# Performance work log

Hardware: AMD Instinct MI355X
Metric: run time of the kernel (lower is better)

Reference implementation:

```python
import jax, jax.numpy as jnp
import numpy as np


def setup_inputs() -> dict:
    key = jax.random.key(0)
    ks = jax.random.split(key, 6)
    B, S, H, F, E = 4, 2048, 1024, 4096, 8
    x = jax.random.normal(ks[0], (B, S, H), dtype=jnp.float32)
    Wr = jax.random.normal(ks[1], (H, E), dtype=jnp.float32) * (1.0 / np.sqrt(H))
    br = jnp.zeros((E,), dtype=jnp.float32)
    W1 = jax.random.normal(ks[2], (E, H, F), dtype=jnp.float32) * (1.0 / np.sqrt(H))
    b1 = jnp.zeros((E, F), dtype=jnp.float32)
    W2 = jax.random.normal(ks[3], (E, F, H), dtype=jnp.float32) * (1.0 / np.sqrt(F))
    b2 = jnp.zeros((E, H), dtype=jnp.float32)
    b_buf = jnp.zeros((E,), dtype=jnp.float32)  # load-balancing bias buffer, zero-init
    return {"x": x, "b_buf": b_buf, "Wr": Wr, "br": br,
            "W1": W1, "b1": b1, "W2": W2, "b2": b2, "k": 2}


def reference(x, b_buf, Wr, br, W1, b1, W2, b2, k):
    # Router
    scores = jnp.einsum('bsh,he->bse', x, Wr) + br          # [B,S,E]
    probs = jax.nn.softmax(scores, axis=-1)
    # load_balancing: expert selection uses biased scores (b_buf pre-update)
    _, expert_id = jax.lax.top_k(probs + b_buf, k)          # [B,S,k] int
    # combine weights use unbiased probs
    p, _ = jax.lax.top_k(probs, k)                          # [B,S,k]
    # Dense-dispatch reference: run every expert MLP on all tokens,
    # then select via one-hot mask (same math as gather/scatter dispatch).
    h1 = jnp.einsum('bsh,ehf->ebsf', x, W1) + b1[:, None, None, :]
    h1 = jax.nn.gelu(h1, approximate=False)                 # torch nn.GELU = exact
    out_e = jnp.einsum('ebsf,efh->ebsh', h1, W2) + b2[:, None, None, :]
    E = W1.shape[0]
    onehot = (expert_id[None, :, :, :] == jnp.arange(E)[:, None, None, None]).astype(x.dtype)  # [E,B,S,k]
    out_k = jnp.einsum('ebsk,ebsh->bskh', onehot, out_e)    # scatter-combine per slot
    w = p / jnp.sum(p, axis=-1, keepdims=True)              # normalize top-k probs
    return jnp.einsum('bsk,bskh->bsh', w, out_k)
```

## Files before the change

### kernel.cpp

```cpp
#include <hip/hip_runtime.h>
#include <stdint.h>

#define NTOK 8192
#define H_ 1024
#define F_ 4096
#define E_ 8
#define VCAP 18432
#define VMBLK 72
#define MT 144
#define NCOMP 16384

using f32x4  = __attribute__((ext_vector_type(4))) float;
using short8 = __attribute__((ext_vector_type(8))) short;

typedef __attribute__((address_space(1))) const uint32_t gu32;
typedef __attribute__((address_space(3))) uint32_t lu32;

__device__ __forceinline__ void glds16(const void* g, void* l) {
  __builtin_amdgcn_global_load_lds((gu32*)g, (lu32*)l, 16, 0, 0);
}

__device__ __forceinline__ ushort f2bf(float f) {
  union { float f; uint32_t u; } v; v.f = f;
  uint32_t r = (v.u + 0x7FFFu + ((v.u >> 16) & 1u)) >> 16;
  return (ushort)r;
}

__device__ __forceinline__ float gelu_t(float x) {
  float u = 0.7978845608028654f * (x + 0.044715f * x * x * x);
  float e = exp2f(u * 2.885390081777927f);
  float th = 1.0f - 2.0f / (1.0f + e);
  return 0.5f * x * (1.0f + th);
}

__global__ void k_init(int* cnt, int* cur, int* tok, float* wl, int* v2c) {
  int i = blockIdx.x * 256 + threadIdx.x;
  if (i < E_) { cnt[i] = 0; cur[i] = 0; }
  if (i < VCAP) { tok[i] = -1; wl[i] = 0.f; v2c[i] = -1; }
}

__global__ __launch_bounds__(256) void k_transcvt(const float* __restrict__ W,
                                                  ushort* __restrict__ WT,
                                                  int R, int C) {
  __shared__ float t[64][65];
  int e = blockIdx.z;
  int c0 = blockIdx.x * 64, r0 = blockIdx.y * 64;
  const float* Wp = W + (size_t)e * R * C;
  ushort* Tp = WT + (size_t)e * R * C;
  int tx = threadIdx.x & 15, ty = threadIdx.x >> 4;
#pragma unroll
  for (int i = 0; i < 4; i++) {
    int lr = ty + i * 16;
    const float4 v = *(const float4*)&Wp[(size_t)(r0 + lr) * C + c0 + tx * 4];
    t[lr][tx * 4 + 0] = v.x; t[lr][tx * 4 + 1] = v.y;
    t[lr][tx * 4 + 2] = v.z; t[lr][tx * 4 + 3] = v.w;
  }
  __syncthreads();
#pragma unroll
  for (int i = 0; i < 4; i++) {
    int lc = ty + i * 16;
    ushort4 o;
    o.x = f2bf(t[tx * 4 + 0][lc]);
    o.y = f2bf(t[tx * 4 + 1][lc]);
    o.z = f2bf(t[tx * 4 + 2][lc]);
    o.w = f2bf(t[tx * 4 + 3][lc]);
    *(ushort4*)&Tp[(size_t)(c0 + lc) * R + r0 + tx * 4] = o;
  }
}

__global__ __launch_bounds__(256) void k_router(const float* __restrict__ x,
                                                const float* __restrict__ Wr,
                                                const float* __restrict__ br,
                                                const float* __restrict__ bbuf,
                                                int* cnt, int* te, float* tw) {
  int wid = threadIdx.x >> 6, lane = threadIdx.x & 63;
  int t = blockIdx.x * 4 + wid;
  const float* xp = x + (size_t)t * H_;
  double acc[E_];
#pragma unroll
  for (int e = 0; e < E_; e++) acc[e] = 0.0;
  for (int j = lane; j < H_; j += 64) {
    float xv = xp[j];
    const float4 w0 = *(const float4*)&Wr[j * 8];
    const float4 w1 = *(const float4*)&Wr[j * 8 + 4];
    acc[0] += (double)xv * (double)w0.x;
    acc[1] += (double)xv * (double)w0.y;
    acc[2] += (double)xv * (double)w0.z;
    acc[3] += (double)xv * (double)w0.w;
    acc[4] += (double)xv * (double)w1.x;
    acc[5] += (double)xv * (double)w1.y;
    acc[6] += (double)xv * (double)w1.z;
    acc[7] += (double)xv * (double)w1.w;
  }
#pragma unroll
  for (int e = 0; e < E_; e++)
    for (int s = 32; s > 0; s >>= 1) acc[e] += __shfl_xor(acc[e], s);
  if (lane == 0) {
    double s[E_], m = -1e300;
    for (int e = 0; e < E_; e++) { s[e] = acc[e] + (double)br[e]; if (s[e] > m) m = s[e]; }
    double pe[E_], sum = 0.0;
    for (int e = 0; e < E_; e++) { pe[e] = exp(s[e] - m); sum += pe[e]; }
    double pr[E_], bb[E_];
    for (int e = 0; e < E_; e++) { pr[e] = pe[e] / sum; bb[e] = pr[e] + (double)bbuf[e]; }
    int e0 = 0;
    for (int e = 1; e < E_; e++) if (bb[e] > bb[e0]) e0 = e;
    int e1 = (e0 == 0) ? 1 : 0;
    for (int e = 0; e < E_; e++) if (e != e0 && bb[e] > bb[e1]) e1 = e;
    int a0 = 0;
    for (int e = 1; e < E_; e++) if (pr[e] > pr[a0]) a0 = e;
    int a1 = (a0 == 0) ? 1 : 0;
    for (int e = 0; e < E_; e++) if (e != a0 && pr[e] > pr[a1]) a1 = e;
    double iv = 1.0 / (pr[a0] + pr[a1]);
    te[t * 2] = e0; te[t * 2 + 1] = e1;
    tw[t * 2] = (float)(pr[a0] * iv); tw[t * 2 + 1] = (float)(pr[a1] * iv);
    atomicAdd(&cnt[e0], 1); atomicAdd(&cnt[e1], 1);
  }
}

__global__ void k_offsets(const int* cnt, int* off, int* coff) {
  if (threadIdx.x == 0 && blockIdx.x == 0) {
    int o = 0, c = 0;
    for (int e = 0; e < E_; e++) {
      off[e] = o; coff[e] = c;
      o += ((cnt[e] + 255) >> 8) << 8;
      c += cnt[e];
    }
    off[E_] = o; coff[E_] = c;
  }
}

__global__ void k_build(const int* __restrict__ te, const float* __restrict__ tw,
                        const int* __restrict__ off, const int* __restrict__ coff,
                        int* cur, int* tok, float* wl, int* v2c, int* ctok) {
  int t = blockIdx.x * 256 + threadIdx.x;
  if (t >= NTOK) return;
#pragma unroll
  for (int s = 0; s < 2; s++) {
    int e = te[t * 2 + s];
    int slot = atomicAdd(&cur[e], 1);
    int vp = off[e] + slot;
    int cp = coff[e] + slot;
    tok[vp] = t; wl[vp] = tw[t * 2 + s]; v2c[vp] = cp; ctok[cp] = t;
  }
}

__global__ __launch_bounds__(256) void k_gather(const float* __restrict__ x,
                                                const int* __restrict__ ctok,
                                                ushort* __restrict__ Xg) {
  int row = blockIdx.x;
  int t = ctok[row];
  const float4* src = (const float4*)(x + (size_t)t * H_);
  ushort4* dst = (ushort4*)(Xg + (size_t)row * H_);
  int i = threadIdx.x;
  float4 v = src[i];
  ushort4 o; o.x = f2bf(v.x); o.y = f2bf(v.y); o.z = f2bf(v.z); o.w = f2bf(v.w);
  dst[i] = o;
}

__global__ void k_zero(float* out) {
  size_t i = (size_t)blockIdx.x * 256 + threadIdx.x;
  float4 z; z.x = 0.f; z.y = 0.f; z.z = 0.f; z.w = 0.f;
  ((float4*)out)[i] = z;
}

template <int MODE>
__global__ __launch_bounds__(256, 4) void k_gemm(const ushort* __restrict__ A,
                                                 const ushort* __restrict__ BT,
                                                 const float* __restrict__ bias,
                                                 ushort* __restrict__ h1,
                                                 float* __restrict__ Out,
                                                 const int* __restrict__ off,
                                                 const int* __restrict__ v2c,
                                                 const int* __restrict__ tok,
                                                 const float* __restrict__ wl,
                                                 int K, int N, int NTe) {
  __shared__ __align__(16) ushort As[128 * 64];
  __shared__ __align__(16) ushort Bs[128 * 64];

  int nwg = gridDim.x;
  int cpx = nwg >> 3;
  int bid = blockIdx.x;
  int lid = (bid & 7) * cpx + (bid >> 3);
  int ng = lid / (MT * 4), r = lid % (MT * 4);
  int m = r >> 2;
  int ne = (ng << 2) + (r & 3);
  int row0 = m << 7;
  if (row0 >= off[E_]) return;
  int e = 0;
  while (off[e + 1] <= row0) e++;
  int n0, k0, nk;
  if (MODE == 0) { n0 = ne << 7; k0 = 0; nk = K >> 6; }
  else           { n0 = (ne >> 1) << 7; k0 = (ne & 1) * (K >> 1); nk = K >> 7; }
  const ushort* Bp = BT + (size_t)e * (size_t)N * (size_t)K;

  int tid = threadIdx.x, lane = tid & 63, w = tid >> 6;
  int wr = w >> 1, wc = w & 1;

  f32x4 acc[4][4];
#pragma unroll
  for (int mm = 0; mm < 4; mm++)
#pragma unroll
    for (int nn = 0; nn < 4; nn++) acc[mm][nn] = (f32x4){0.f, 0.f, 0.f, 0.f};

  int urow = (w << 3) + (lane >> 3);
  int sc = (lane & 7) ^ (urow & 7);
  const char *aP0, *aP1, *aP2, *aP3, *bP0, *bP1, *bP2, *bP3;
  {
    size_t kb = (size_t)k0 * 2 + (size_t)sc * 16;
    int c0 = v2c[row0 + 0 * 32 + urow];  if (c0 < 0) c0 = 0;
    int c1 = v2c[row0 + 1 * 32 + urow];  if (c1 < 0) c1 = 0;
    int c2 = v2c[row0 + 2 * 32 + urow];  if (c2 < 0) c2 = 0;
    int c3 = v2c[row0 + 3 * 32 + urow];  if (c3 < 0) c3 = 0;
    aP0 = (const char*)(A + (size_t)c0 * K) + kb;
    aP1 = (const char*)(A + (size_t)c1 * K) + kb;
    aP2 = (const char*)(A + (size_t)c2 * K) + kb;
    aP3 = (const char*)(A + (size_t)c3 * K) + kb;
    bP0 = (const char*)(Bp + (size_t)(n0 + 0 * 32 + urow) * K) + kb;
    bP1 = (const char*)(Bp + (size_t)(n0 + 1 * 32 + urow) * K) + kb;
    bP2 = (const char*)(Bp + (size_t)(n0 + 2 * 32 + urow) * K) + kb;
    bP3 = (const char*)(Bp + (size_t)(n0 + 3 * 32 + urow) * K) + kb;
  }

  int fr = lane & 15, fq = lane >> 4;
  int frs = fr & 7;

  for (int kk = 0; kk < nk; ++kk) {
    size_t kbo = (size_t)kk * 128;
    if (kk) __syncthreads();
    glds16(aP0 + kbo, (char*)As + 0 * 4096 + (w << 10));
    glds16(bP0 + kbo, (char*)Bs + 0 * 4096 + (w << 10));
    glds16(aP1 + kbo, (char*)As + 1 * 4096 + (w << 10));
    glds16(bP1 + kbo, (char*)Bs + 1 * 4096 + (w << 10));
    glds16(aP2 + kbo, (char*)As + 2 * 4096 + (w << 10));
    glds16(bP2 + kbo, (char*)Bs + 2 * 4096 + (w << 10));
    glds16(aP3 + kbo, (char*)As + 3 * 4096 + (w << 10));
    glds16(bP3 + kbo, (char*)Bs + 3 * 4096 + (w << 10));
    __syncthreads();
#pragma unroll
    for (int ks = 0; ks < 2; ++ks) {
      short8 af[4], bf[4];
      int kc = (((ks << 2) + fq) ^ frs) << 3;
#pragma unroll
      for (int i = 0; i < 4; ++i)
        af[i] = *(const short8*)&As[((wr << 6) + i * 16 + fr) * 64 + kc];
#pragma unroll
      for (int i = 0; i < 4; ++i)
        bf[i] = *(const short8*)&Bs[((wc << 6) + i * 16 + fr) * 64 + kc];
#pragma unroll
      for (int mm = 0; mm < 4; ++mm)
#pragma unroll
        for (int nn = 0; nn < 4; ++nn)
          acc[mm][nn] = __builtin_amdgcn_mfma_f32_16x16x32_bf16(af[mm], bf[nn], acc[mm][nn], 0, 0, 0);
    }
  }

  const float* bp = bias + (size_t)e * N;
  int cb = n0 + (wc << 6);
  if (MODE == 0) {
#pragma unroll
    for (int mm = 0; mm < 4; mm++) {
#pragma unroll
      for (int j = 0; j < 4; j++) {
        int vr = row0 + (wr << 6) + mm * 16 + (fq << 2) + j;
        int cr = v2c[vr];
        if (cr < 0) continue;
        ushort* hp = h1 + (size_t)cr * N + cb;
#pragma unroll
        for (int nn = 0; nn < 4; nn++) {
          float v = acc[mm][nn][j] + bp[cb + nn * 16 + fr];
          hp[nn * 16 + fr] = f2bf(gelu_t(v));
        }
      }
    }
  } else {
    bool addb = (k0 == 0);
#pragma unroll
    for (int mm = 0; mm < 4; mm++) {
#pragma unroll
      for (int j = 0; j < 4; j++) {
        int vr = row0 + (wr << 6) + mm * 16 + (fq << 2) + j;
        int t2 = tok[vr];
        if (t2 < 0) continue;
        float wgt = wl[vr];
#pragma unroll
        for (int nn = 0; nn < 4; nn++) {
          int c = cb + nn * 16 + fr;
          float v = acc[mm][nn][j] + (addb ? bp[c] : 0.f);
          atomicAdd(&Out[(size_t)t2 * (size_t)N + c], wgt * v);
        }
      }
    }
  }
}

extern "C" void kernel_launch(void* const* d_in, const int* in_sizes, int n_in,
                              void* d_out, int out_size, void* d_ws, size_t ws_size,
                              hipStream_t stream) {
  (void)in_sizes; (void)n_in; (void)out_size; (void)ws_size;
  const float* x    = (const float*)d_in[0];
  const float* bbuf = (const float*)d_in[1];
  const float* Wr   = (const float*)d_in[2];
  const float* br   = (const float*)d_in[3];
  const float* W1   = (const float*)d_in[4];
  const float* b1   = (const float*)d_in[5];
  const float* W2   = (const float*)d_in[6];
  const float* b2   = (const float*)d_in[7];
  float* out = (float*)d_out;

  char* ws = (char*)d_ws;
  ushort* W1T = (ushort*)ws;
  ushort* W2T = (ushort*)(ws + 67108864);
  ushort* Xg  = (ushort*)(ws + 134217728);
  ushort* h1  = (ushort*)(ws + 167772160);
  char* meta  = ws + 301989888;
  int*   cnt  = (int*)(meta);
  int*   off  = (int*)(meta + 64);
  int*   coff = (int*)(meta + 128);
  int*   cur  = (int*)(meta + 192);
  int*   te   = (int*)(meta + 256);
  float* tw   = (float*)(meta + 65792);
  int*   tok  = (int*)(meta + 131328);
  float* wl   = (float*)(meta + 205056);
  int*   v2c  = (int*)(meta + 278784);
  int*   ctok = (int*)(meta + 352512);

  k_init<<<VMBLK, 256, 0, stream>>>(cnt, cur, tok, wl, v2c);
  k_transcvt<<<dim3(F_ / 64, H_ / 64, E_), 256, 0, stream>>>(W1, W1T, H_, F_);
  k_transcvt<<<dim3(H_ / 64, F_ / 64, E_), 256, 0, stream>>>(W2, W2T, F_, H_);
  k_router<<<NTOK / 4, 256, 0, stream>>>(x, Wr, br, bbuf, cnt, te, tw);
  k_offsets<<<1, 64, 0, stream>>>(cnt, off, coff);
  k_build<<<NTOK / 256, 256, 0, stream>>>(te, tw, off, coff, cur, tok, wl, v2c, ctok);
  k_gather<<<NCOMP, 256, 0, stream>>>(x, ctok, Xg);
  k_zero<<<(NTOK * H_ / 4) / 256, 256, 0, stream>>>(out);
  k_gemm<0><<<32 * MT, 256, 0, stream>>>(Xg, W1T, b1, h1, nullptr,
                                         off, v2c, nullptr, nullptr,
                                         H_, F_, 32);
  k_gemm<1><<<16 * MT, 256, 0, stream>>>(h1, W2T, b2, nullptr, out,
                                         off, v2c, tok, wl,
                                         F_, H_, 16);
}
```

Measured before the change: 887.9 us.

## Double-buffer LDS tiles with async global-to-LDS prefetch in expert GEMM

```diff
diff --git a/kernel.cpp b/kernel.cpp
--- a/kernel.cpp
+++ b/kernel.cpp
@@ -174,8 +174,8 @@
                                                  const int* __restrict__ tok,
                                                  const float* __restrict__ wl,
                                                  int K, int N, int NTe) {
-  __shared__ __align__(16) ushort As[128 * 64];
-  __shared__ __align__(16) ushort Bs[128 * 64];
+  __shared__ __align__(16) ushort As[2][128 * 32];
+  __shared__ __align__(16) ushort Bs[2][128 * 32];
 
   int nwg = gridDim.x;
   int cpx = nwg >> 3;
@@ -189,8 +189,8 @@
   int e = 0;
   while (off[e + 1] <= row0) e++;
   int n0, k0, nk;
-  if (MODE == 0) { n0 = ne << 7; k0 = 0; nk = K >> 6; }
-  else           { n0 = (ne >> 1) << 7; k0 = (ne & 1) * (K >> 1); nk = K >> 7; }
+  if (MODE == 0) { n0 = ne << 7; k0 = 0; nk = K >> 5; }
+  else           { n0 = (ne >> 1) << 7; k0 = (ne & 1) * (K >> 1); nk = K >> 6; }
   const ushort* Bp = BT + (size_t)e * (size_t)N * (size_t)K;
 
   int tid = threadIdx.x, lane = tid & 63, w = tid >> 6;
@@ -202,57 +202,54 @@
 #pragma unroll
     for (int nn = 0; nn < 4; nn++) acc[mm][nn] = (f32x4){0.f, 0.f, 0.f, 0.f};
 
-  int urow = (w << 3) + (lane >> 3);
-  int sc = (lane & 7) ^ (urow & 7);
-  const char *aP0, *aP1, *aP2, *aP3, *bP0, *bP1, *bP2, *bP3;
+  int srow = lane >> 2;
+  int sc = (lane & 3) ^ ((lane >> 3) & 3);
+  const char *aP0, *aP1, *bP0, *bP1;
   {
     size_t kb = (size_t)k0 * 2 + (size_t)sc * 16;
-    int c0 = v2c[row0 + 0 * 32 + urow];  if (c0 < 0) c0 = 0;
-    int c1 = v2c[row0 + 1 * 32 + urow];  if (c1 < 0) c1 = 0;
-    int c2 = v2c[row0 + 2 * 32 + urow];  if (c2 < 0) c2 = 0;
-    int c3 = v2c[row0 + 3 * 32 + urow];  if (c3 < 0) c3 = 0;
+    int c0 = v2c[row0 + (w << 5) + srow];        if (c0 < 0) c0 = 0;
+    int c1 = v2c[row0 + (w << 5) + 16 + srow];   if (c1 < 0) c1 = 0;
     aP0 = (const char*)(A + (size_t)c0 * K) + kb;
     aP1 = (const char*)(A + (size_t)c1 * K) + kb;
-    aP2 = (const char*)(A + (size_t)c2 * K) + kb;
-    aP3 = (const char*)(A + (size_t)c3 * K) + kb;
-    bP0 = (const char*)(Bp + (size_t)(n0 + 0 * 32 + urow) * K) + kb;
-    bP1 = (const char*)(Bp + (size_t)(n0 + 1 * 32 + urow) * K) + kb;
-    bP2 = (const char*)(Bp + (size_t)(n0 + 2 * 32 + urow) * K) + kb;
-    bP3 = (const char*)(Bp + (size_t)(n0 + 3 * 32 + urow) * K) + kb;
+    bP0 = (const char*)(Bp + (size_t)(n0 + (w << 5) + srow) * K) + kb;
+    bP1 = (const char*)(Bp + (size_t)(n0 + (w << 5) + 16 + srow) * K) + kb;
   }
 
   int fr = lane & 15, fq = lane >> 4;
-  int frs = fr & 7;
-
-  for (int kk = 0; kk < nk; ++kk) {
-    size_t kbo = (size_t)kk * 128;
-    if (kk) __syncthreads();
-    glds16(aP0 + kbo, (char*)As + 0 * 4096 + (w << 10));
-    glds16(bP0 + kbo, (char*)Bs + 0 * 4096 + (w << 10));
-    glds16(aP1 + kbo, (char*)As + 1 * 4096 + (w << 10));
-    glds16(bP1 + kbo, (char*)Bs + 1 * 4096 + (w << 10));
-    glds16(aP2 + kbo, (char*)As + 2 * 4096 + (w << 10));
-    glds16(bP2 + kbo, (char*)Bs + 2 * 4096 + (w << 10));
-    glds16(aP3 + kbo, (char*)As + 3 * 4096 + (w << 10));
-    glds16(bP3 + kbo, (char*)Bs + 3 * 4096 + (w << 10));
+  int kc = (fq ^ ((fr >> 1) & 3)) << 3;
+
+#define STAGE(T, bb) do {                                                    \
+    size_t kbo = (size_t)(T) * 64;                                           \
+    glds16(aP0 + kbo, (char*)As + (bb) * 8192 + (w << 11));                  \
+    glds16(aP1 + kbo, (char*)As + (bb) * 8192 + (w << 11) + 1024);           \
+    glds16(bP0 + kbo, (char*)Bs + (bb) * 8192 + (w << 11));                  \
+    glds16(bP1 + kbo, (char*)Bs + (bb) * 8192 + (w << 11) + 1024);           \
+  } while (0)
+
+  STAGE(0, 0);
+  STAGE(1, 1);
+
+  for (int T = 0; T < nk; ++T) {
+    int bb = T & 1;
+    if (T + 1 < nk) asm volatile("s_waitcnt vmcnt(4)" ::: "memory");
+    else            asm volatile("s_waitcnt vmcnt(0)" ::: "memory");
+    __builtin_amdgcn_s_barrier();
+    short8 af[4], bf[4];
+#pragma unroll
+    for (int i = 0; i < 4; ++i)
+      af[i] = *(const short8*)&As[bb][((wr << 6) + i * 16 + fr) * 32 + kc];
+#pragma unroll
+    for (int i = 0; i < 4; ++i)
+      bf[i] = *(const short8*)&Bs[bb][((wc << 6) + i * 16 + fr) * 32 + kc];
+#pragma unroll
+    for (int mm = 0; mm < 4; ++mm)
+#pragma unroll
+      for (int nn = 0; nn < 4; ++nn)
+        acc[mm][nn] = __builtin_amdgcn_mfma_f32_16x16x32_bf16(af[mm], bf[nn], acc[mm][nn], 0, 0, 0);
     __syncthreads();
-#pragma unroll
-    for (int ks = 0; ks < 2; ++ks) {
-      short8 af[4], bf[4];
-      int kc = (((ks << 2) + fq) ^ frs) << 3;
-#pragma unroll
-      for (int i = 0; i < 4; ++i)
-        af[i] = *(const short8*)&As[((wr << 6) + i * 16 + fr) * 64 + kc];
-#pragma unroll
-      for (int i = 0; i < 4; ++i)
-        bf[i] = *(const short8*)&Bs[((wc << 6) + i * 16 + fr) * 64 + kc];
-#pragma unroll
-      for (int mm = 0; mm < 4; ++mm)
-#pragma unroll
-        for (int nn = 0; nn < 4; ++nn)
-          acc[mm][nn] = __builtin_amdgcn_mfma_f32_16x16x32_bf16(af[mm], bf[nn], acc[mm][nn], 0, 0, 0);
-    }
-  }
+    if (T + 2 < nk) STAGE(T + 2, bb);
+  }
+#undef STAGE
 
   const float* bp = bias + (size_t)e * N;
   int cb = n0 + (wc << 6);
```

Measured after the change: 917.0 us. 1.03x slower.
